# Performance work log

Measured on AMD Instinct MI355X. Metric: run time of the kernel, lower is better.

The kernel has to match this reference:

```python
import jax, jax.numpy as jnp
import numpy as np

NHEAD, HD, ITERS = 8, 32, 6


def _layernorm(x, g, b, eps=1e-5):
    mu = jnp.mean(x, axis=-1, keepdims=True)
    var = jnp.mean((x - mu) ** 2, axis=-1, keepdims=True)
    return g * (x - mu) / jnp.sqrt(var + eps) + b


def _msa1(x, ax, WQ, bQ, WK, bK, WV, bV, WO, bO):
    # ring (sliding-window, size 3) attention + relay node as 4th key/value
    B, L, H = x.shape
    q = (x @ WQ + bQ).reshape(B, L, NHEAD, HD)
    k = (x @ WK + bK).reshape(B, L, NHEAD, HD)
    ak = (ax @ WK + bK).reshape(B, 1, NHEAD, 1, HD)   # relay key
    av = (ax @ WV + bV).reshape(B, 1, NHEAD, 1, HD)   # relay value
    padk = jnp.pad(k, ((0, 0), (1, 1), (0, 0), (0, 0)))
    wins = jnp.stack([padk[:, t:L + t] for t in range(3)], axis=3)  # [B,L,nh,3,hd]
    ak_b = jnp.broadcast_to(ak, (B, L, NHEAD, 1, HD))
    av_b = jnp.broadcast_to(av, (B, L, NHEAD, 1, HD))
    keys = jnp.concatenate([ak_b, wins], axis=3)   # [B,L,nh,4,hd]
    # NOTE: faithful to source bug: window VALUES come from k (pad_v = F.pad(k,...))
    vals = jnp.concatenate([av_b, wins], axis=3)
    scores = jnp.einsum('blnd,blnkd->blnk', q, keys) / np.sqrt(HD).astype(np.float32)
    alphas = jax.nn.softmax(scores, axis=-1)
    att = jnp.einsum('blnk,blnkd->blnd', alphas, vals).reshape(B, L, NHEAD * HD)
    return att @ WO + bO


def _msa2(x, y, WQ, bQ, WK, bK, WV, bV, WO, bO):
    # relay attends over [relay; nodes]; mask arg is ignored in the original
    B, L1, H = y.shape
    q = (x @ WQ + bQ).reshape(B, NHEAD, HD)
    k = (y @ WK + bK).reshape(B, L1, NHEAD, HD)
    v = (y @ WV + bV).reshape(B, L1, NHEAD, HD)
    scores = jnp.einsum('bnd,blnd->bnl', q, k) / np.sqrt(HD).astype(np.float32)
    alphas = jax.nn.softmax(scores, axis=-1)
    att = jnp.einsum('bnl,blnd->bnd', alphas, v).reshape(B, NHEAD * HD)
    return att @ WO + bO


def setup_inputs() -> dict:
    key = jax.random.key(0)
    ks = jax.random.split(key, 32)
    B, L, H, V, E, I = 32, 512, 256, 32000, 300, 6

    def rn(k, shape, s=0.05):
        return jax.random.normal(k, shape, jnp.float32) * s

    inp = {
        'data': jax.random.randint(ks[0], (B, L), 0, V),
        'emb': rn(ks[1], (V, E), 0.1),
        'emb_fc_W': rn(ks[2], (E, H)),
        'emb_fc_b': jnp.zeros((H,), jnp.float32),
        'pos_emb': rn(ks[3], (1000, H), 0.02),
        'ln_g': jnp.ones((I, H), jnp.float32),
        'ln_b': jnp.zeros((I, H), jnp.float32),
    }
    names = ['r_WQ', 'r_WK', 'r_WV', 'r_WO', 's_WQ', 's_WK', 's_WV', 's_WO']
    for j, n in enumerate(names):
        inp[n] = rn(ks[4 + j], (I, H, H))
        inp[n.replace('W', 'b')] = rn(ks[12 + j], (I, H), 0.01)
    return inp


def reference(data, emb, emb_fc_W, emb_fc_b, pos_emb, ln_g, ln_b,
              r_WQ, r_bQ, r_WK, r_bK, r_WV, r_bV, r_WO, r_bO,
              s_WQ, s_bQ, s_WK, s_bK, s_WV, s_bV, s_WO, s_bO):
    B, L = data.shape
    mask = (data == 1)
    e = emb[data]                                  # [B,L,nemb]
    P = pos_emb[:L][None]                          # [1,L,H]
    x0 = e @ emb_fc_W + emb_fc_b + P               # [B,L,H]
    nodes = x0
    relay = jnp.mean(x0, axis=1)                   # [B,H]
    for i in range(ITERS):
        ax = relay
        n_ln = _layernorm(nodes, ln_g[i], ln_b[i])
        nodes = nodes + jax.nn.leaky_relu(
            _msa1(n_ln, ax, r_WQ[i], r_bQ[i], r_WK[i], r_bK[i],
                  r_WV[i], r_bV[i], r_WO[i], r_bO[i]))
        y = jnp.concatenate([relay[:, None, :], nodes], axis=1)
        relay = jax.nn.leaky_relu(
            _msa2(relay, y, s_WQ[i], s_bQ[i], s_WK[i], s_bK[i],
                  s_WV[i], s_bV[i], s_WO[i], s_bO[i]))
        nodes = jnp.where(mask[:, :, None], 0.0, nodes)
    rep = 0.5 * jnp.max(nodes, axis=1) + 0.5 * relay
    return rep
```

## Files before the change

### kernel.cpp

```cpp
#include <hip/hip_runtime.h>
#include <stdint.h>

typedef __bf16 bf16x8 __attribute__((ext_vector_type(8)));
typedef unsigned short ushort8 __attribute__((ext_vector_type(8)));
typedef float floatx4 __attribute__((ext_vector_type(4)));

__device__ __forceinline__ unsigned short f2b(float f) {
    unsigned int u = __builtin_bit_cast(unsigned int, f);
    u += 0x7fffu + ((u >> 16) & 1u);
    return (unsigned short)(u >> 16);
}
__device__ __forceinline__ float b2f(unsigned short u) {
    union { unsigned int i; float f; } x; x.i = ((unsigned int)u) << 16; return x.f;
}
__device__ __forceinline__ void gl_lds16(const unsigned short* g, unsigned short* l) {
    __builtin_amdgcn_global_load_lds(
        (const __attribute__((address_space(1))) unsigned int*)g,
        (__attribute__((address_space(3))) unsigned int*)l, 16, 0, 0);
}

#define SCALE_QK 0.17677669529663687f

__global__ __launch_bounds__(256) void transpose_many(const float* __restrict__ w0,
                                                      const float* __restrict__ w1,
                                                      const float* __restrict__ w2,
                                                      const float* __restrict__ w3,
                                                      const float* __restrict__ w4,
                                                      const float* __restrict__ wemb,
                                                      unsigned short* __restrict__ out,
                                                      unsigned short* __restrict__ outEmb,
                                                      float* __restrict__ relayAcc) {
    __shared__ float tile[64][65];
    int m = blockIdx.y;
    int tid = threadIdx.x;
    if (m == 30) {
#pragma unroll
        for (int i = 0; i < 20; i++) {
            int e = i * 4096 + blockIdx.x * 256 + tid;
            int n = e / 320, k = e - n * 320;
            outEmb[e] = (k < 300) ? f2b(wemb[k * 256 + n]) : (unsigned short)0;
        }
        if (blockIdx.x == 0) {
#pragma unroll
            for (int j = 0; j < 32; j++) relayAcc[j * 256 + tid] = 0.f;
        }
        return;
    }
    int fam = m / 6, it = m % 6;
    const float* src =
        (fam == 0 ? w0 : fam == 1 ? w1 : fam == 2 ? w2 : fam == 3 ? w3 : w4) + it * 65536;
    unsigned short* dst = out + (size_t)(it * 5 + fam) * 65536;
    int k0 = (blockIdx.x & 3) * 64, n0 = (blockIdx.x >> 2) * 64;
    int rg = tid >> 6, cl = tid & 63;
#pragma unroll
    for (int i = 0; i < 16; i++) {
        int kl = rg * 16 + i;
        tile[kl][cl] = src[(k0 + kl) * 256 + n0 + cl];
    }
    __syncthreads();
#pragma unroll
    for (int i = 0; i < 16; i++) {
        int nl = rg * 16 + i;
        dst[(n0 + nl) * 256 + k0 + cl] = f2b(tile[cl][nl]);
    }
}

__global__ void gather_emb(const int* __restrict__ data,
                           const float* __restrict__ emb,
                           unsigned short* __restrict__ apad) {
    int row = blockIdx.x;
    int tok = data[row];
    const float* er = emb + (size_t)tok * 300;
    for (int c = threadIdx.x; c < 320; c += 256)
        apad[(size_t)row * 320 + c] = (c < 300) ? f2b(er[c]) : (unsigned short)0;
}

template <int EPI, int KDIM, int NC>
__global__ __launch_bounds__(256) void gemm_k(const unsigned short* __restrict__ A,
                                              const unsigned short* __restrict__ Bt,
                                              const float* __restrict__ bias0,
                                              const float* __restrict__ bias1,
                                              float* __restrict__ outF,
                                              unsigned short* __restrict__ outB0,
                                              unsigned short* __restrict__ outB1,
                                              const float* __restrict__ pos,
                                              const int* __restrict__ dmask,
                                              int applyMask,
                                              float* __restrict__ relayAcc) {
    constexpr int G = KDIM / 8;
    __shared__ unsigned short Asm[64 * KDIM];
    __shared__ unsigned short Bsm[64 * KDIM];
    const int tid = threadIdx.x;
    const int wave = tid >> 6, lane = tid & 63;
    const int wm = (wave >> 1) * 32, wn = (wave & 1) * 32;
    const int quad = lane >> 4, l16 = lane & 15;
    const int id = blockIdx.x;
    const int xcd = id & 7, t = id >> 3;
    const int cIdx = t % NC, rhi = t / NC;
    const int rowBase = (rhi * 8 + xcd) * 64, colBase = cIdx * 64;
    {
        const unsigned short* gbA = A + (size_t)(rowBase + wave * 16) * KDIM;
        const unsigned short* gbB = Bt + (size_t)(colBase + wave * 16) * KDIM;
        unsigned short* lbA = Asm + wave * 16 * KDIM;
        unsigned short* lbB = Bsm + wave * 16 * KDIM;
#pragma unroll
        for (int c = 0; c < G / 4; c++) {
            int gi = c * 64 + lane;
            int rl = gi / G, sl = gi - rl * G;
            int sg = sl ^ (rl & 7);
            gl_lds16(gbA + rl * KDIM + sg * 8, lbA + gi * 8);
            gl_lds16(gbB + rl * KDIM + sg * 8, lbB + gi * 8);
        }
    }
    __syncthreads();

    floatx4 acc[2][2] = {};
    const int mr0 = wm + l16, mr1 = wm + 16 + l16;
    const int nr0 = wn + l16, nr1 = wn + 16 + l16;
#pragma unroll
    for (int ks = 0; ks < KDIM / 32; ks++) {
        int g = ks * 4 + quad;
        bf16x8 af0 = __builtin_bit_cast(bf16x8, *(const ushort8*)&Asm[mr0 * KDIM + ((g ^ (mr0 & 7)) * 8)]);
        bf16x8 af1 = __builtin_bit_cast(bf16x8, *(const ushort8*)&Asm[mr1 * KDIM + ((g ^ (mr1 & 7)) * 8)]);
        bf16x8 bf0 = __builtin_bit_cast(bf16x8, *(const ushort8*)&Bsm[nr0 * KDIM + ((g ^ (nr0 & 7)) * 8)]);
        bf16x8 bf1 = __builtin_bit_cast(bf16x8, *(const ushort8*)&Bsm[nr1 * KDIM + ((g ^ (nr1 & 7)) * 8)]);
        acc[0][0] = __builtin_amdgcn_mfma_f32_16x16x32_bf16(af0, bf0, acc[0][0], 0, 0, 0);
        acc[0][1] = __builtin_amdgcn_mfma_f32_16x16x32_bf16(af0, bf1, acc[0][1], 0, 0, 0);
        acc[1][0] = __builtin_amdgcn_mfma_f32_16x16x32_bf16(af1, bf0, acc[1][0], 0, 0, 0);
        acc[1][1] = __builtin_amdgcn_mfma_f32_16x16x32_bf16(af1, bf1, acc[1][1], 0, 0, 0);
    }
    if (EPI == 0) {
        const int group = colBase >> 8;
        const float* bias = group ? bias1 : bias0;
        unsigned short* obf = group ? outB1 : outB0;
        unsigned short* tile = Asm;
        __syncthreads();
#pragma unroll
        for (int tm = 0; tm < 2; tm++) {
#pragma unroll
            for (int tn = 0; tn < 2; tn++) {
                int lcl = wn + tn * 16 + l16;
                float bv = bias[(colBase & 255) + lcl];
#pragma unroll
                for (int r = 0; r < 4; r++) {
                    int rl = wm + tm * 16 + quad * 4 + r;
                    tile[rl * 72 + lcl] = f2b(acc[tm][tn][r] + bv);
                }
            }
        }
        __syncthreads();
#pragma unroll
        for (int j = 0; j < 2; j++) {
            int c = j * 256 + tid;
            int rl = c >> 3, c8 = c & 7;
            ushort8 v = *(const ushort8*)&tile[rl * 72 + c8 * 8];
            *(ushort8*)(obf + (size_t)(rowBase + rl) * 256 + (colBase & 255) + c8 * 8) = v;
        }
    } else {
#pragma unroll
        for (int tm = 0; tm < 2; tm++) {
#pragma unroll
            for (int tn = 0; tn < 2; tn++) {
                int col = colBase + wn + tn * 16 + l16;
                int lc = col & 255;
                float bv = bias0[lc];
                float cs = 0.f;
#pragma unroll
                for (int r = 0; r < 4; r++) {
                    int row = rowBase + wm + tm * 16 + quad * 4 + r;
                    float c = acc[tm][tn][r] + bv;
                    size_t o = (size_t)row * 256 + lc;
                    if (EPI == 1) {
                        float v = c > 0.f ? c : 0.01f * c;
                        float base = outF[o];
                        if (applyMask && dmask[row] == 1) base = 0.f;
                        float rr = base + v;
                        outF[o] = rr;
                        outB0[o] = f2b(rr);
                    } else {
                        float v = c + pos[(row & 511) * 256 + lc];
                        outF[o] = v;
                        cs += v;
                    }
                }
                if (EPI == 2) {
                    cs += __shfl_xor(cs, 16);
                    cs += __shfl_xor(cs, 32);
                    if (quad == 0)
                        atomicAdd(&relayAcc[(rowBase >> 9) * 256 + lc], cs * (1.f / 512.f));
                }
            }
        }
    }
}

__global__ __launch_bounds__(256) void ln_k(const float* __restrict__ nodes,
                                            const float* __restrict__ g,
                                            const float* __restrict__ bb,
                                            unsigned short* __restrict__ out,
                                            const int* __restrict__ dmask,
                                            int applyMask) {
    int wave = threadIdx.x >> 6, lane = threadIdx.x & 63;
    int row = blockIdx.x * 4 + wave;
    float4 x = *(const float4*)(nodes + (size_t)row * 256 + lane * 4);
    if (applyMask && dmask[row] == 1) { x.x = 0.f; x.y = 0.f; x.z = 0.f; x.w = 0.f; }
    float s = x.x + x.y + x.z + x.w;
    float q = x.x * x.x + x.y * x.y + x.z * x.z + x.w * x.w;
#pragma unroll
    for (int o = 32; o; o >>= 1) { s += __shfl_xor(s, o); q += __shfl_xor(q, o); }
    float mu = s * (1.f / 256.f);
    float var = q * (1.f / 256.f) - mu * mu;
    float inv = rsqrtf(fmaxf(var, 0.f) + 1e-5f);
    float4 gv = *(const float4*)(g + lane * 4);
    float4 bv = *(const float4*)(bb + lane * 4);
    ushort4 r4;
    r4.x = f2b(gv.x * (x.x - mu) * inv + bv.x);
    r4.y = f2b(gv.y * (x.y - mu) * inv + bv.y);
    r4.z = f2b(gv.z * (x.z - mu) * inv + bv.z);
    r4.w = f2b(gv.w * (x.w - mu) * inv + bv.w);
    *(ushort4*)(out + (size_t)row * 256 + lane * 4) = r4;
}

__global__ __launch_bounds__(1024) void relay5(const float* __restrict__ relay,
                       const float* __restrict__ rWK, const float* __restrict__ rbK,
                       const float* __restrict__ rWV, const float* __restrict__ rbV,
                       const float* __restrict__ sWQ, const float* __restrict__ sbQ,
                       const float* __restrict__ sWK, const float* __restrict__ sbK,
                       const float* __restrict__ sWV, const float* __restrict__ sbV,
                       float* __restrict__ AK, float* __restrict__ AV,
                       float* __restrict__ Q2, float* __restrict__ RK2, float* __restrict__ RV2) {
    __shared__ float r[256];
    __shared__ float part[1024];
    int b = blockIdx.x, fam = blockIdx.y, t = threadIdx.x;
    if (t < 256) r[t] = relay[b * 256 + t];
    __syncthreads();
    const float* W; const float* bi; float* o;
    switch (fam) {
        case 0: W = rWK; bi = rbK; o = AK; break;
        case 1: W = rWV; bi = rbV; o = AV; break;
        case 2: W = sWQ; bi = sbQ; o = Q2; break;
        case 3: W = sWK; bi = sbK; o = RK2; break;
        default: W = sWV; bi = sbV; o = RV2; break;
    }
    int col = t & 255, kc = t >> 8;
    float s = 0.f;
    for (int e = kc * 64; e < kc * 64 + 64; e++) s += r[e] * W[e * 256 + col];
    part[t] = s;
    __syncthreads();
    if (kc == 0)
        o[b * 256 + col] = part[col] + part[256 + col] + part[512 + col] + part[768 + col] + bi[col];
}

__global__ __launch_bounds__(256) void attn1_k(const unsigned short* __restrict__ q,
                                               const unsigned short* __restrict__ k,
                                               const float* __restrict__ ak,
                                               const float* __restrict__ av,
                                               unsigned short* __restrict__ att) {
    int tid = threadIdx.x;
    int nb = (blockIdx.x & 7) * 512 + (blockIdx.x >> 3);
    int row = nb * 4 + (tid >> 6);
    int b = row >> 9, l = row & 511;
    int t = tid & 63;
    size_t o = (size_t)row * 256 + t * 4;
    ushort4 z4; z4.x = z4.y = z4.z = z4.w = 0;
    ushort4 q4 = *(const ushort4*)(q + o);
    ushort4 k04 = *(const ushort4*)(k + o);
    ushort4 km4 = (l > 0) ? *(const ushort4*)(k + o - 256) : z4;
    ushort4 kp4 = (l < 511) ? *(const ushort4*)(k + o + 256) : z4;
    float4 akv = *(const float4*)(ak + b * 256 + t * 4);
    float4 avv = *(const float4*)(av + b * 256 + t * 4);
    float qv0 = b2f(q4.x), qv1 = b2f(q4.y), qv2 = b2f(q4.z), qv3 = b2f(q4.w);
    float k00 = b2f(k04.x), k01 = b2f(k04.y), k02 = b2f(k04.z), k03 = b2f(k04.w);
    float km0 = b2f(km4.x), km1 = b2f(km4.y), km2 = b2f(km4.z), km3 = b2f(km4.w);
    float kp0 = b2f(kp4.x), kp1 = b2f(kp4.y), kp2 = b2f(kp4.z), kp3 = b2f(kp4.w);
    float s0 = qv0 * akv.x + qv1 * akv.y + qv2 * akv.z + qv3 * akv.w;
    float s1 = qv0 * km0 + qv1 * km1 + qv2 * km2 + qv3 * km3;
    float s2 = qv0 * k00 + qv1 * k01 + qv2 * k02 + qv3 * k03;
    float s3 = qv0 * kp0 + qv1 * kp1 + qv2 * kp2 + qv3 * kp3;
#pragma unroll
    for (int off = 4; off; off >>= 1) {
        s0 += __shfl_xor(s0, off);
        s1 += __shfl_xor(s1, off);
        s2 += __shfl_xor(s2, off);
        s3 += __shfl_xor(s3, off);
    }
    s0 *= SCALE_QK; s1 *= SCALE_QK; s2 *= SCALE_QK; s3 *= SCALE_QK;
    float m = fmaxf(fmaxf(s0, s1), fmaxf(s2, s3));
    float e0 = __expf(s0 - m), e1 = __expf(s1 - m), e2 = __expf(s2 - m), e3 = __expf(s3 - m);
    float iZ = 1.f / (e0 + e1 + e2 + e3);
    ushort4 r4;
    r4.x = f2b((e0 * avv.x + e1 * km0 + e2 * k00 + e3 * kp0) * iZ);
    r4.y = f2b((e0 * avv.y + e1 * km1 + e2 * k01 + e3 * kp1) * iZ);
    r4.z = f2b((e0 * avv.z + e1 * km2 + e2 * k02 + e3 * kp2) * iZ);
    r4.w = f2b((e0 * avv.w + e1 * km3 + e2 * k03 + e3 * kp3) * iZ);
    *(ushort4*)(att + o) = r4;
}

__global__ __launch_bounds__(512) void attn2_k(const float* __restrict__ q2,
                                               const unsigned short* __restrict__ k2,
                                               const unsigned short* __restrict__ v2,
                                               const float* __restrict__ rk2,
                                               const float* __restrict__ rv2,
                                               float* __restrict__ att2) {
    __shared__ float sc[513];
    __shared__ float qs[32];
    __shared__ float red[16];
    __shared__ float red2[512];
    int bn = blockIdx.x;
    int b = bn >> 3, n = bn & 7;
    int t = threadIdx.x;
    if (t < 32) qs[t] = q2[b * 256 + n * 32 + t];
    __syncthreads();
    float lmax = -1e30f;
    for (int li = t; li < 513; li += 512) {
        float d = 0.f;
        if (li == 0) {
            const float* kr = rk2 + b * 256 + n * 32;
#pragma unroll 8
            for (int j = 0; j < 32; j++) d += qs[j] * kr[j];
        } else {
            const ushort8* kr8 = (const ushort8*)(k2 + ((size_t)(b * 512 + li - 1) * 256 + n * 32));
#pragma unroll
            for (int jj = 0; jj < 4; jj++) {
                ushort8 v = kr8[jj];
                d += qs[jj * 8 + 0] * b2f(v[0]) + qs[jj * 8 + 1] * b2f(v[1]) +
                     qs[jj * 8 + 2] * b2f(v[2]) + qs[jj * 8 + 3] * b2f(v[3]) +
                     qs[jj * 8 + 4] * b2f(v[4]) + qs[jj * 8 + 5] * b2f(v[5]) +
                     qs[jj * 8 + 6] * b2f(v[6]) + qs[jj * 8 + 7] * b2f(v[7]);
            }
        }
        d *= SCALE_QK;
        sc[li] = d;
        lmax = fmaxf(lmax, d);
    }
#pragma unroll
    for (int o = 32; o; o >>= 1) lmax = fmaxf(lmax, __shfl_xor(lmax, o));
    if ((t & 63) == 0) red[t >> 6] = lmax;
    __syncthreads();
    float m = red[0];
#pragma unroll
    for (int i = 1; i < 8; i++) m = fmaxf(m, red[i]);
    float lsum = 0.f;
    for (int li = t; li < 513; li += 512) {
        float e = __expf(sc[li] - m);
        sc[li] = e;
        lsum += e;
    }
#pragma unroll
    for (int o = 32; o; o >>= 1) lsum += __shfl_xor(lsum, o);
    if ((t & 63) == 0) red[8 + (t >> 6)] = lsum;
    __syncthreads();
    float Z = red[8];
#pragma unroll
    for (int i = 9; i < 16; i++) Z += red[i];
    int d_ = t & 31, g_ = t >> 5;
    float acc = 0.f;
    for (int li = g_; li < 513; li += 16) {
        if (li == 0) {
            acc += sc[0] * rv2[b * 256 + n * 32 + d_];
        } else {
            acc += sc[li] * b2f(v2[(size_t)(b * 512 + li - 1) * 256 + n * 32 + d_]);
        }
    }
    red2[t] = acc;
    __syncthreads();
    if (t < 32) {
        float s = 0.f;
#pragma unroll
        for (int g = 0; g < 16; g++) s += red2[g * 32 + t];
        att2[b * 256 + n * 32 + t] = s / Z;
    }
}

__global__ __launch_bounds__(1024) void relay_out2(const float* __restrict__ att2,
                           const float* __restrict__ WO, const float* __restrict__ bO,
                           float* __restrict__ relay) {
    __shared__ float r[256];
    __shared__ float part[1024];
    int b = blockIdx.x, t = threadIdx.x;
    if (t < 256) r[t] = att2[b * 256 + t];
    __syncthreads();
    int col = t & 255, kc = t >> 8;
    float s = 0.f;
    for (int e = kc * 64; e < kc * 64 + 64; e++) s += r[e] * WO[e * 256 + col];
    part[t] = s;
    __syncthreads();
    if (kc == 0) {
        float tot = part[col] + part[256 + col] + part[512 + col] + part[768 + col] + bO[col];
        relay[b * 256 + col] = tot > 0.f ? tot : 0.01f * tot;
    }
}

__global__ void rep_part(const float* __restrict__ nodes, const int* __restrict__ dmask,
                         float* __restrict__ part) {
    int b = blockIdx.x, c = blockIdx.y, h = threadIdx.x;
    const float* p = nodes + ((size_t)b * 512 + c * 32) * 256 + h;
    const int* dd = dmask + b * 512 + c * 32;
    float m = -1e30f;
    for (int l = 0; l < 32; l++) {
        float v = (dd[l] == 1) ? 0.f : p[l * 256];
        m = fmaxf(m, v);
    }
    part[(b * 16 + c) * 256 + h] = m;
}
__global__ void rep_comb(const float* __restrict__ part, const float* __restrict__ relay,
                         float* __restrict__ out) {
    int b = blockIdx.x, h = threadIdx.x;
    float m = -1e30f;
    for (int c = 0; c < 16; c++) m = fmaxf(m, part[(b * 16 + c) * 256 + h]);
    out[b * 256 + h] = 0.5f * m + 0.5f * relay[b * 256 + h];
}

extern "C" void kernel_launch(void* const* d_in, const int* in_sizes, int n_in,
                              void* d_out, int out_size, void* d_ws, size_t ws_size,
                              hipStream_t stream) {
    const int* data = (const int*)d_in[0];
    const float* emb = (const float*)d_in[1];
    const float* emb_fc_W = (const float*)d_in[2];
    const float* emb_fc_b = (const float*)d_in[3];
    const float* pos_emb = (const float*)d_in[4];
    const float* ln_g = (const float*)d_in[5];
    const float* ln_b = (const float*)d_in[6];
    const float* r_WQ = (const float*)d_in[7];
    const float* r_bQ = (const float*)d_in[8];
    const float* r_WK = (const float*)d_in[9];
    const float* r_bK = (const float*)d_in[10];
    const float* r_WV = (const float*)d_in[11];
    const float* r_bV = (const float*)d_in[12];
    const float* r_WO = (const float*)d_in[13];
    const float* r_bO = (const float*)d_in[14];
    const float* s_WQ = (const float*)d_in[15];
    const float* s_bQ = (const float*)d_in[16];
    const float* s_WK = (const float*)d_in[17];
    const float* s_bK = (const float*)d_in[18];
    const float* s_WV = (const float*)d_in[19];
    const float* s_bV = (const float*)d_in[20];
    const float* s_WO = (const float*)d_in[21];
    const float* s_bO = (const float*)d_in[22];

    char* w = (char*)d_ws;
    size_t off = 0;
    auto alloc = [&](size_t bytes) -> char* {
        char* p = w + off;
        off += (bytes + 255) & ~(size_t)255;
        return p;
    };
    float* RELAY = (float*)alloc(8192 * 4);
    float* AK = (float*)alloc(8192 * 4);
    float* AV = (float*)alloc(8192 * 4);
    float* Q2 = (float*)alloc(8192 * 4);
    float* RK2 = (float*)alloc(8192 * 4);
    float* RV2 = (float*)alloc(8192 * 4);
    float* ATT2 = (float*)alloc(8192 * 4);
    float* PART = (float*)alloc((size_t)32 * 16 * 256 * 4);
    unsigned short* WTE = (unsigned short*)alloc((size_t)256 * 320 * 2);
    unsigned short* WT = (unsigned short*)alloc((size_t)30 * 65536 * 2);
    float* NODES = (float*)alloc((size_t)16384 * 256 * 4);
    unsigned short* NLN = (unsigned short*)alloc((size_t)16384 * 256 * 2);
    unsigned short* Qb = (unsigned short*)alloc((size_t)16384 * 256 * 2);
    unsigned short* Kb16 = (unsigned short*)alloc((size_t)16384 * 256 * 2);
    unsigned short* NBF = (unsigned short*)alloc((size_t)16384 * 320 * 2);
    unsigned short* AEMB = NBF;
    unsigned short* ATT = NLN;
    unsigned short* K2b = Qb;
    unsigned short* V2b = Kb16;

    transpose_many<<<dim3(16, 31), 256, 0, stream>>>(r_WQ, r_WK, r_WO, s_WK, s_WV,
                                                     emb_fc_W, WT, WTE, RELAY);
    gather_emb<<<16384, 256, 0, stream>>>(data, emb, AEMB);
    gemm_k<2, 320, 4><<<1024, 256, 0, stream>>>(AEMB, WTE, emb_fc_b, nullptr,
                                                NODES, nullptr, nullptr, pos_emb,
                                                nullptr, 0, RELAY);

    for (int i = 0; i < 6; i++) {
        const unsigned short* wQK = WT + (size_t)(i * 5 + 0) * 65536;
        const unsigned short* wO = WT + (size_t)(i * 5 + 2) * 65536;
        const unsigned short* wKV2 = WT + (size_t)(i * 5 + 3) * 65536;

        ln_k<<<4096, 256, 0, stream>>>(NODES, ln_g + i * 256, ln_b + i * 256, NLN, data, i > 0);
        gemm_k<0, 256, 8><<<2048, 256, 0, stream>>>(NLN, wQK, r_bQ + i * 256, r_bK + i * 256,
                                                    nullptr, Qb, Kb16, nullptr, nullptr, 0,
                                                    nullptr);
        relay5<<<dim3(32, 5), 1024, 0, stream>>>(RELAY,
                                                 r_WK + (size_t)i * 65536, r_bK + i * 256,
                                                 r_WV + (size_t)i * 65536, r_bV + i * 256,
                                                 s_WQ + (size_t)i * 65536, s_bQ + i * 256,
                                                 s_WK + (size_t)i * 65536, s_bK + i * 256,
                                                 s_WV + (size_t)i * 65536, s_bV + i * 256,
                                                 AK, AV, Q2, RK2, RV2);
        attn1_k<<<4096, 256, 0, stream>>>(Qb, Kb16, AK, AV, ATT);
        gemm_k<1, 256, 4><<<1024, 256, 0, stream>>>(ATT, wO, r_bO + i * 256, nullptr,
                                                    NODES, NBF, nullptr, nullptr, data, i > 0,
                                                    nullptr);
        gemm_k<0, 256, 8><<<2048, 256, 0, stream>>>(NBF, wKV2, s_bK + i * 256, s_bV + i * 256,
                                                    nullptr, K2b, V2b, nullptr, nullptr, 0,
                                                    nullptr);
        attn2_k<<<256, 512, 0, stream>>>(Q2, K2b, V2b, RK2, RV2, ATT2);
        relay_out2<<<32, 1024, 0, stream>>>(ATT2, s_WO + (size_t)i * 65536, s_bO + i * 256, RELAY);
    }
    rep_part<<<dim3(32, 16), 256, 0, stream>>>(NODES, data, PART);
    rep_comb<<<32, 256, 0, stream>>>(PART, RELAY, (float*)d_out);
}
```

Baseline: 696.7 us.

## Fold relay projections and final max-reduction into existing GEMM and relay kernels

```diff
diff --git a/kernel.cpp b/kernel.cpp
--- a/kernel.cpp
+++ b/kernel.cpp
@@ -20,6 +20,17 @@
 }
 
 #define SCALE_QK 0.17677669529663687f
+
+struct Extra {
+    int mode;
+    const float* relay;
+    const float* W[5];
+    const float* bvec[5];
+    float* out5[5];
+    const float* nodes;
+    const int* dmask;
+    float* part;
+};
 
 __global__ __launch_bounds__(256) void transpose_many(const float* __restrict__ w0,
                                                       const float* __restrict__ w1,
@@ -86,15 +97,44 @@
                                               const float* __restrict__ pos,
                                               const int* __restrict__ dmask,
                                               int applyMask,
-                                              float* __restrict__ relayAcc) {
+                                              float* __restrict__ relayAcc,
+                                              Extra ex) {
     constexpr int G = KDIM / 8;
+    constexpr int NT = 8 * NC * 32;
     __shared__ unsigned short Asm[64 * KDIM];
     __shared__ unsigned short Bsm[64 * KDIM];
     const int tid = threadIdx.x;
+    const int id = blockIdx.x;
+    if (id >= NT) {
+        int e = id - NT;
+        if (ex.mode == 1) {
+            float* rs = (float*)Asm;
+            rs[tid] = ex.relay[e * 256 + tid];
+            __syncthreads();
+#pragma unroll
+            for (int f = 0; f < 5; f++) {
+                const float* W = ex.W[f];
+                float s = 0.f;
+#pragma unroll 8
+                for (int k = 0; k < 256; k++) s += rs[k] * W[k * 256 + tid];
+                ex.out5[f][e * 256 + tid] = s + ex.bvec[f][tid];
+            }
+        } else {
+            int b = e >> 4, c = e & 15;
+            const float* p = ex.nodes + ((size_t)b * 512 + c * 32) * 256 + tid;
+            const int* dd = ex.dmask + b * 512 + c * 32;
+            float m = -1e30f;
+            for (int l = 0; l < 32; l++) {
+                float v = (dd[l] == 1) ? 0.f : p[l * 256];
+                m = fmaxf(m, v);
+            }
+            ex.part[(b * 16 + c) * 256 + tid] = m;
+        }
+        return;
+    }
     const int wave = tid >> 6, lane = tid & 63;
     const int wm = (wave >> 1) * 32, wn = (wave & 1) * 32;
     const int quad = lane >> 4, l16 = lane & 15;
-    const int id = blockIdx.x;
     const int xcd = id & 7, t = id >> 3;
     const int cIdx = t % NC, rhi = t / NC;
     const int rowBase = (rhi * 8 + xcd) * 64, colBase = cIdx * 64;
@@ -219,36 +259,6 @@
     r4.z = f2b(gv.z * (x.z - mu) * inv + bv.z);
     r4.w = f2b(gv.w * (x.w - mu) * inv + bv.w);
     *(ushort4*)(out + (size_t)row * 256 + lane * 4) = r4;
-}
-
-__global__ __launch_bounds__(1024) void relay5(const float* __restrict__ relay,
-                       const float* __restrict__ rWK, const float* __restrict__ rbK,
-                       const float* __restrict__ rWV, const float* __restrict__ rbV,
-                       const float* __restrict__ sWQ, const float* __restrict__ sbQ,
-                       const float* __restrict__ sWK, const float* __restrict__ sbK,
-                       const float* __restrict__ sWV, const float* __restrict__ sbV,
-                       float* __restrict__ AK, float* __restrict__ AV,
-                       float* __restrict__ Q2, float* __restrict__ RK2, float* __restrict__ RV2) {
-    __shared__ float r[256];
-    __shared__ float part[1024];
-    int b = blockIdx.x, fam = blockIdx.y, t = threadIdx.x;
-    if (t < 256) r[t] = relay[b * 256 + t];
-    __syncthreads();
-    const float* W; const float* bi; float* o;
-    switch (fam) {
-        case 0: W = rWK; bi = rbK; o = AK; break;
-        case 1: W = rWV; bi = rbV; o = AV; break;
-        case 2: W = sWQ; bi = sbQ; o = Q2; break;
-        case 3: W = sWK; bi = sbK; o = RK2; break;
-        default: W = sWV; bi = sbV; o = RV2; break;
-    }
-    int col = t & 255, kc = t >> 8;
-    float s = 0.f;
-    for (int e = kc * 64; e < kc * 64 + 64; e++) s += r[e] * W[e * 256 + col];
-    part[t] = s;
-    __syncthreads();
-    if (kc == 0)
-        o[b * 256 + col] = part[col] + part[256 + col] + part[512 + col] + part[768 + col] + bi[col];
 }
 
 __global__ __launch_bounds__(256) void attn1_k(const unsigned short* __restrict__ q,
@@ -374,41 +384,31 @@
 
 __global__ __launch_bounds__(1024) void relay_out2(const float* __restrict__ att2,
                            const float* __restrict__ WO, const float* __restrict__ bO,
-                           float* __restrict__ relay) {
+                           float* __restrict__ relay,
+                           const float* __restrict__ part,
+                           float* __restrict__ outp,
+                           int doFinal) {
     __shared__ float r[256];
-    __shared__ float part[1024];
+    __shared__ float partl[1024];
     int b = blockIdx.x, t = threadIdx.x;
     if (t < 256) r[t] = att2[b * 256 + t];
     __syncthreads();
     int col = t & 255, kc = t >> 8;
     float s = 0.f;
     for (int e = kc * 64; e < kc * 64 + 64; e++) s += r[e] * WO[e * 256 + col];
-    part[t] = s;
+    partl[t] = s;
     __syncthreads();
     if (kc == 0) {
-        float tot = part[col] + part[256 + col] + part[512 + col] + part[768 + col] + bO[col];
-        relay[b * 256 + col] = tot > 0.f ? tot : 0.01f * tot;
-    }
-}
-
-__global__ void rep_part(const float* __restrict__ nodes, const int* __restrict__ dmask,
-                         float* __restrict__ part) {
-    int b = blockIdx.x, c = blockIdx.y, h = threadIdx.x;
-    const float* p = nodes + ((size_t)b * 512 + c * 32) * 256 + h;
-    const int* dd = dmask + b * 512 + c * 32;
-    float m = -1e30f;
-    for (int l = 0; l < 32; l++) {
-        float v = (dd[l] == 1) ? 0.f : p[l * 256];
-        m = fmaxf(m, v);
-    }
-    part[(b * 16 + c) * 256 + h] = m;
-}
-__global__ void rep_comb(const float* __restrict__ part, const float* __restrict__ relay,
-                         float* __restrict__ out) {
-    int b = blockIdx.x, h = threadIdx.x;
-    float m = -1e30f;
-    for (int c = 0; c < 16; c++) m = fmaxf(m, part[(b * 16 + c) * 256 + h]);
-    out[b * 256 + h] = 0.5f * m + 0.5f * relay[b * 256 + h];
+        float tot = partl[col] + partl[256 + col] + partl[512 + col] + partl[768 + col] + bO[col];
+        tot = tot > 0.f ? tot : 0.01f * tot;
+        relay[b * 256 + col] = tot;
+        if (doFinal) {
+            float m = -1e30f;
+#pragma unroll
+            for (int c = 0; c < 16; c++) m = fmaxf(m, part[(b * 16 + c) * 256 + col]);
+            outp[b * 256 + col] = 0.5f * m + 0.5f * tot;
+        }
+    }
 }
 
 extern "C" void kernel_launch(void* const* d_in, const int* in_sizes, int n_in,
@@ -465,39 +465,54 @@
     unsigned short* K2b = Qb;
     unsigned short* V2b = Kb16;
 
+    Extra exNone = {};
+    exNone.mode = 0;
+
     transpose_many<<<dim3(16, 31), 256, 0, stream>>>(r_WQ, r_WK, r_WO, s_WK, s_WV,
                                                      emb_fc_W, WT, WTE, RELAY);
     gather_emb<<<16384, 256, 0, stream>>>(data, emb, AEMB);
     gemm_k<2, 320, 4><<<1024, 256, 0, stream>>>(AEMB, WTE, emb_fc_b, nullptr,
                                                 NODES, nullptr, nullptr, pos_emb,
-                                                nullptr, 0, RELAY);
+                                                nullptr, 0, RELAY, exNone);
 
     for (int i = 0; i < 6; i++) {
         const unsigned short* wQK = WT + (size_t)(i * 5 + 0) * 65536;
         const unsigned short* wO = WT + (size_t)(i * 5 + 2) * 65536;
         const unsigned short* wKV2 = WT + (size_t)(i * 5 + 3) * 65536;
 
+        Extra exR = {};
+        exR.mode = 1;
+        exR.relay = RELAY;
+        exR.W[0] = r_WK + (size_t)i * 65536; exR.bvec[0] = r_bK + i * 256; exR.out5[0] = AK;
+        exR.W[1] = r_WV + (size_t)i * 65536; exR.bvec[1] = r_bV + i * 256; exR.out5[1] = AV;
+        exR.W[2] = s_WQ + (size_t)i * 65536; exR.bvec[2] = s_bQ + i * 256; exR.out5[2] = Q2;
+        exR.W[3] = s_WK + (size_t)i * 65536; exR.bvec[3] = s_bK + i * 256; exR.out5[3] = RK2;
+        exR.W[4] = s_WV + (size_t)i * 65536; exR.bvec[4] = s_bV + i * 256; exR.out5[4] = RV2;
+
         ln_k<<<4096, 256, 0, stream>>>(NODES, ln_g + i * 256, ln_b + i * 256, NLN, data, i > 0);
-        gemm_k<0, 256, 8><<<2048, 256, 0, stream>>>(NLN, wQK, r_bQ + i * 256, r_bK + i * 256,
+        gemm_k<0, 256, 8><<<2080, 256, 0, stream>>>(NLN, wQK, r_bQ + i * 256, r_bK + i * 256,
                                                     nullptr, Qb, Kb16, nullptr, nullptr, 0,
-                                                    nullptr);
-        relay5<<<dim3(32, 5), 1024, 0, stream>>>(RELAY,
-                                                 r_WK + (size_t)i * 65536, r_bK + i * 256,
-                                                 r_WV + (size_t)i * 65536, r_bV + i * 256,
-                                                 s_WQ + (size_t)i * 65536, s_bQ + i * 256,
-                                                 s_WK + (size_t)i * 65536, s_bK + i * 256,
-                                                 s_WV + (size_t)i * 65536, s_bV + i * 256,
-                                                 AK, AV, Q2, RK2, RV2);
+                                                    nullptr, exR);
         attn1_k<<<4096, 256, 0, stream>>>(Qb, Kb16, AK, AV, ATT);
         gemm_k<1, 256, 4><<<1024, 256, 0, stream>>>(ATT, wO, r_bO + i * 256, nullptr,
                                                     NODES, NBF, nullptr, nullptr, data, i > 0,
-                                                    nullptr);
-        gemm_k<0, 256, 8><<<2048, 256, 0, stream>>>(NBF, wKV2, s_bK + i * 256, s_bV + i * 256,
-                                                    nullptr, K2b, V2b, nullptr, nullptr, 0,
-                                                    nullptr);
+                                                    nullptr, exNone);
+        if (i == 5) {
+            Extra exP = {};
+            exP.mode = 2;
+            exP.nodes = NODES;
+            exP.dmask = data;
+            exP.part = PART;
+            gemm_k<0, 256, 8><<<2560, 256, 0, stream>>>(NBF, wKV2, s_bK + i * 256, s_bV + i * 256,
+                                                        nullptr, K2b, V2b, nullptr, nullptr, 0,
+                                                        nullptr, exP);
+        } else {
+            gemm_k<0, 256, 8><<<2048, 256, 0, stream>>>(NBF, wKV2, s_bK + i * 256, s_bV + i * 256,
+                                                        nullptr, K2b, V2b, nullptr, nullptr, 0,
+                                                        nullptr, exNone);
+        }
         attn2_k<<<256, 512, 0, stream>>>(Q2, K2b, V2b, RK2, RV2, ATT2);
-        relay_out2<<<32, 1024, 0, stream>>>(ATT2, s_WO + (size_t)i * 65536, s_bO + i * 256, RELAY);
-    }
-    rep_part<<<dim3(32, 16), 256, 0, stream>>>(NODES, data, PART);
-    rep_comb<<<32, 256, 0, stream>>>(PART, RELAY, (float*)d_out);
-}
+        relay_out2<<<32, 1024, 0, stream>>>(ATT2, s_WO + (size_t)i * 65536, s_bO + i * 256, RELAY,
+                                            PART, (float*)d_out, i == 5 ? 1 : 0);
+    }
+}
```

Measured after the change: 975.8 us. +40.1%, slower.
